# Performance work log

Measured on AMD Instinct MI355X. Metric: run time of the kernel, lower is better.

Reference implementation:

```python
import jax, jax.numpy as jnp
import numpy as np
from jax import lax

# Dense-equivalent of the spconv net: SubMConv/SparseConv with stride 1 and
# size-preserving padding on a dense input reduce to ordinary conv2d.
# Layer chain: (1->64,k1) PReLU (64->256,k3) PReLU (256->512,k3) PReLU
# (512->256,k3) PReLU (256->64,k3) PReLU (64->1,k3) PReLU, then symmetrize.

CHANS = [(1, 64, 1), (64, 256, 3), (256, 512, 3), (512, 256, 3), (256, 64, 3), (64, 1, 3)]


def _conv(x, w, b, k):
    pad = ((k // 2, k // 2), (k // 2, k // 2))
    y = lax.conv_general_dilated(x, w, window_strides=(1, 1), padding=pad,
                                 dimension_numbers=('NCHW', 'OIHW', 'NCHW'))
    return y + b[None, :, None, None]


def _prelu(x, a):
    return jnp.where(x >= 0, x, a * x)


def setup_inputs() -> dict:
    key = jax.random.key(0)
    keys = jax.random.split(key, 1 + 2 * len(CHANS))
    inp = {'A': jax.random.normal(keys[0], (1, 1, 512, 512), dtype=jnp.float32)}
    for i, (cin, cout, k) in enumerate(CHANS):
        fan_in = cin * k * k
        std = 1.0 / np.sqrt(fan_in)
        inp[f'w{i}'] = jax.random.normal(keys[1 + 2 * i], (cout, cin, k, k), dtype=jnp.float32) * std
        inp[f'b{i}'] = jax.random.normal(keys[2 + 2 * i], (cout,), dtype=jnp.float32) * std
        inp[f'p{i}'] = jnp.full((1,), 0.25, dtype=jnp.float32)  # PReLU default weight
    return inp


def reference(A, w0, b0, p0, w1, b1, p1, w2, b2, p2, w3, b3, p3, w4, b4, p4, w5, b5, p5):
    params = [(w0, b0, p0), (w1, b1, p1), (w2, b2, p2), (w3, b3, p3), (w4, b4, p4), (w5, b5, p5)]
    x = A
    for (w, b, p), (_, _, k) in zip(params, CHANS):
        x = _prelu(_conv(x, w, b, k), p)
    # make_symmetric: average with transpose over the spatial (matrix) dims
    return 0.5 * (x + jnp.swapaxes(x, -1, -2))
```

## Files before the change

kernel.cpp:

```cpp
#include <hip/hip_runtime.h>
#include <hip/hip_bf16.h>
#include <stdint.h>

typedef __bf16 bf16_t;
typedef __bf16 bf16x8 __attribute__((ext_vector_type(8)));
typedef float  f32x4  __attribute__((ext_vector_type(4)));

#define HP 514
#define AS1 __attribute__((address_space(1)))
#define AS3 __attribute__((address_space(3)))

__device__ __forceinline__ bf16_t f2bf(float f) { return (bf16_t)f; }

__global__ void l0_kernel(const float* __restrict__ A, const float* __restrict__ w0,
                          const float* __restrict__ b0, const float* __restrict__ p0,
                          bf16_t* __restrict__ X0)
{
    int idx = blockIdx.x * 256 + threadIdx.x;
    if (idx >= HP * HP * 64) return;
    int c   = idx & 63;
    int pix = idx >> 6;
    int py = pix / HP, px = pix - py * HP;
    float v = 0.f;
    if (py >= 1 && py <= 512 && px >= 1 && px <= 512) {
        float a = A[(py - 1) * 512 + (px - 1)];
        v = fmaf(w0[c], a, b0[c]);
        v = v >= 0.f ? v : p0[0] * v;
    }
    X0[idx] = f2bf(v);
}

__global__ void zero_rows_kernel(bf16_t* __restrict__ buf, int C, int r0, int n)
{
    int idx = blockIdx.x * 256 + threadIdx.x;
    int rowsz = HP * C;
    if (idx >= n * rowsz) return;
    int r = idx / rowsz, j = idx - r * rowsz;
    buf[(size_t)(r0 + r) * rowsz + j] = f2bf(0.f);
}

__global__ void zero_cols_kernel(bf16_t* __restrict__ buf, int C, int R)
{
    int idx = blockIdx.x * 256 + threadIdx.x;
    if (idx >= R * 2 * C) return;
    int r = idx / (2 * C);
    int t = idx - r * 2 * C;
    int col = (t < C) ? 0 : 513;
    int c = t % C;
    buf[((size_t)r * HP + col) * C + c] = f2bf(0.f);
}

__global__ void wtrans_kernel(const float* __restrict__ w, bf16_t* __restrict__ wt,
                              int COUT, int CIN)
{
    int idx = blockIdx.x * 256 + threadIdx.x;
    if (idx >= COUT * CIN * 9) return;
    int G    = COUT / 16;
    int j    = idx & 7;
    int l    = (idx >> 3) & 63;
    int t    = idx >> 9;
    int gabs = t % G;
    int t2   = t / G;
    int tap  = t2 % 9;
    int ci   = t2 / 9;
    int cout = gabs * 16 + (l & 15);
    int cin  = ci * 32 + (l >> 4) * 8 + j;
    wt[idx] = f2bf(w[(cout * CIN + cin) * 9 + tap]);
}

template<int CIN, int COUT, int BN>
__global__ __launch_bounds__(256, 3)
void conv3x3_kernel(const bf16_t* __restrict__ in, const bf16_t* __restrict__ wt,
                    const float* __restrict__ bias, const float* __restrict__ alpha,
                    bf16_t* __restrict__ out,
                    int n_rows, int in_off, int in_alloc, int out_off)
{
    constexpr int G      = COUT / 16;
    constexpr int NT     = BN / 32;
    constexpr int NC     = CIN / 32;
    constexpr int AUNITS = 18 * 10 * 4;
    constexpr int APAD   = 768;
    constexpr int ASLAB  = APAD * 8;
    __shared__ __align__(16) bf16_t As[2 * ASLAB];

    const int tid  = threadIdx.x;
    const int lane = tid & 63;
    const int wave = tid >> 6;
    const int lm   = lane & 15;
    const int quad = lane >> 4;
    const int wave_m = wave >> 1;
    const int wave_n = wave & 1;

    const int bid  = blockIdx.x + 64 * (blockIdx.y + gridDim.y * blockIdx.z);
    const int nwg  = 64 * gridDim.y * gridDim.z;
    const int sid  = (bid & 7) * (nwg >> 3) + (bid >> 3);
    const int sx   = sid & 63;
    const int tzy  = sid >> 6;
    const int szb  = tzy % gridDim.z;
    const int syb  = tzy / gridDim.z;

    const int x0 = sx * 8;
    const int y0 = syb * 16;
    const int zb = szb;
    const int gb_blk = zb * (BN / 16);

    int a_srcb[3];
    #pragma unroll
    for (int it = 0; it < 3; ++it) {
        int u  = it * 256 + tid;
        int uu = u < AUNITS ? u : AUNITS - 1;
        int qq = uu & 3, px = (uu >> 2) % 10, r = uu / 40;
        int q  = (qq - (px >> 1)) & 3;
        int grow = in_off + y0 + r;
        grow = grow < 0 ? 0 : (grow >= in_alloc ? in_alloc - 1 : grow);
        a_srcb[it] = (grow * HP + x0 + px) * CIN + q * 8;
    }

    const int pxb = lm & 7, pyb = lm >> 3;
    int sw[3];
    #pragma unroll
    for (int dx = 0; dx < 3; ++dx)
        sw[dx] = ((quad + ((pxb + dx) >> 1)) & 3) * 8;
    int addrA0[4];
    #pragma unroll
    for (int mt = 0; mt < 4; ++mt)
        addrA0[mt] = ((wave_m * 8 + mt * 2 + pyb) * 40 + pxb * 4) * 8;

    auto stageA = [&](int cc, int abuf) {
        #pragma unroll
        for (int it = 0; it < 3; ++it) {
            const bf16_t* src = in + a_srcb[it] + cc;
            bf16_t* dst = As + abuf * ASLAB + (it * 256 + wave * 64) * 8;
            __builtin_amdgcn_global_load_lds((AS1 void*)src, (AS3 void*)dst, 16, 0, 0);
        }
    };
    auto loadB = [&](int ft, bf16x8* b) {
        const bf16_t* base = wt + ((size_t)ft * G + gb_blk + wave_n * NT) * 512 + lane * 8;
        #pragma unroll
        for (int nt = 0; nt < NT; ++nt)
            b[nt] = *(const bf16x8*)(base + nt * 512);
    };
    auto readA = [&](int ab, int tap, bf16x8* a) {
        const int dy = tap / 3, dx = tap - dy * 3;
        const int shift = (dy * 40 + dx * 4) * 8 + sw[dx];
        #pragma unroll
        for (int mt = 0; mt < 4; ++mt)
            a[mt] = *(const bf16x8*)(As + ab * ASLAB + addrA0[mt] + shift);
    };

    f32x4 acc[4][NT] = {};
    bf16x8 breg[2][NT];
    bf16x8 areg[2][4];

    stageA(0, 0);
    loadB(0, breg[0]);
    __syncthreads();
    readA(0, 0, areg[0]);

    for (int cp = 0; cp < NC / 2; ++cp) {
        const bool morecp = (cp + 1 < NC / 2);
        const int fb = cp * 18;
        #pragma unroll
        for (int rf = 0; rf < 18; ++rf) {
            if (rf < 17 || morecp)
                loadB(fb + rf + 1, breg[(rf + 1) & 1]);
            if (rf == 0)            stageA((2 * cp + 1) * 32, 1);
            if (rf == 9 && morecp)  stageA((2 * cp + 2) * 32, 0);
            if (rf != 8 && rf != 17)
                readA((rf + 1) >= 9 ? 1 : 0, (rf + 1) % 9, areg[(rf + 1) & 1]);

            __builtin_amdgcn_s_setprio(1);
            #pragma unroll
            for (int mt = 0; mt < 4; ++mt)
                #pragma unroll
                for (int nt = 0; nt < NT; ++nt)
                    acc[mt][nt] = __builtin_amdgcn_mfma_f32_16x16x32_bf16(
                        areg[rf & 1][mt], breg[rf & 1][nt], acc[mt][nt], 0, 0, 0);
            __builtin_amdgcn_s_setprio(0);

            if (rf == 8) {
                __syncthreads();
                readA(1, 0, areg[1]);
            }
            if (rf == 17 && morecp) {
                __syncthreads();
                readA(0, 0, areg[0]);
            }
        }
    }

    const float al = alpha[0];
    #pragma unroll
    for (int nt = 0; nt < NT; ++nt) {
        const int n = zb * BN + wave_n * (BN / 2) + nt * 16 + lm;
        const float bv = bias[n];
        #pragma unroll
        for (int mt = 0; mt < 4; ++mt) {
            f32x4 v = acc[mt][nt];
            #pragma unroll
            for (int r = 0; r < 4; ++r) {
                int m  = wave_m * 64 + mt * 16 + quad * 4 + r;
                int py = m >> 3, px = m & 7;
                int ly = y0 + py;
                if (ly < n_rows) {
                    float f = v[r] + bv;
                    f = f >= 0.f ? f : al * f;
                    out[((size_t)(out_off + ly) * HP + (x0 + px + 1)) * COUT + n] = f2bf(f);
                }
            }
        }
    }
}

__device__ __forceinline__ float conv64_at(const bf16_t* __restrict__ X,
                                           const float* __restrict__ wsh,
                                           int y, int x, float bv)
{
    float acc = bv;
    #pragma unroll
    for (int dy = 0; dy < 3; ++dy) {
        #pragma unroll
        for (int dx = 0; dx < 3; ++dx) {
            const bf16x8* p = (const bf16x8*)(X + ((size_t)(y + dy) * HP + (x + dx)) * 64);
            const float* wf = wsh + (dy * 3 + dx) * 64;
            #pragma unroll
            for (int j = 0; j < 8; ++j) {
                bf16x8 v = p[j];
                #pragma unroll
                for (int k = 0; k < 8; ++k)
                    acc = fmaf((float)v[k], wf[j * 8 + k], acc);
            }
        }
    }
    return acc;
}

__global__ __launch_bounds__(256)
void l5_strip_kernel(const bf16_t* __restrict__ B4, const bf16_t* __restrict__ wt5,
                     const float* __restrict__ b5, const float* __restrict__ p5,
                     float* __restrict__ T, int abs_row0)
{
    __shared__ float wsh[9 * 64];
    for (int i = threadIdx.x; i < 576; i += 256) wsh[i] = (float)wt5[i];
    __syncthreads();
    int idx = blockIdx.x * 256 + threadIdx.x;
    int ly = idx >> 9, x = idx & 511;
    float bv = b5[0], al = p5[0];
    float t = conv64_at(B4, wsh, ly, x, bv);
    t = t >= 0.f ? t : al * t;
    T[(size_t)(abs_row0 + ly) * 512 + x] = t;
}

__global__ void wtrans5_kernel(const float* __restrict__ w, bf16_t* __restrict__ wt)
{
    int idx = blockIdx.x * 256 + threadIdx.x;
    if (idx >= 9 * 64) return;
    int cin = idx % 64, tap = idx / 64;
    wt[idx] = f2bf(w[cin * 9 + tap]);
}

__global__ __launch_bounds__(256)
void sym_kernel(const float* __restrict__ T, float* __restrict__ out)
{
    int idx = blockIdx.x * 256 + threadIdx.x;
    int y = idx >> 9, x = idx & 511;
    out[idx] = 0.5f * (T[idx] + T[x * 512 + y]);
}

extern "C" void kernel_launch(void* const* d_in, const int* in_sizes, int n_in,
                              void* d_out, int out_size, void* d_ws, size_t ws_size,
                              hipStream_t stream)
{
    const float* A = (const float*)d_in[0];
    const float *w[6], *b[6], *p[6];
    for (int i = 0; i < 6; ++i) {
        w[i] = (const float*)d_in[1 + 3 * i];
        b[i] = (const float*)d_in[2 + 3 * i];
        p[i] = (const float*)d_in[3 + 3 * i];
    }

    auto footprint = [](long long S) -> size_t {
        auto al = [](size_t v) { return (v + 255) & ~(size_t)255; };
        size_t t = 0;
        t += al((size_t)HP * HP * 64 * 2);
        t += al((size_t)(S + 8) * HP * 256 * 2);
        t += al((size_t)(S + 6) * HP * 512 * 2);
        t += al((size_t)(S + 2) * HP * 64 * 2);
        t += al((size_t)512 * 512 * 4);
        t += al((size_t)9 * 256 * 64 * 2);
        t += al((size_t)9 * 512 * 256 * 2);
        t += al((size_t)9 * 256 * 512 * 2);
        t += al((size_t)9 * 64 * 256 * 2);
        t += al((size_t)9 * 64 * 2);
        return t;
    };
    const int cand[6] = {512, 256, 128, 64, 32, 16};
    int S = 16;
    for (int i = 0; i < 6; ++i)
        if (footprint(cand[i]) <= ws_size) { S = cand[i]; break; }
    const int nStrips = 512 / S;

    char* ws = (char*)d_ws;
    size_t off = 0;
    auto carve = [&](size_t bytes) -> void* {
        void* r = ws + off;
        off += (bytes + 255) & ~(size_t)255;
        return r;
    };
    bf16_t* X0  = (bf16_t*)carve((size_t)HP * HP * 64 * 2);
    bf16_t* B1  = (bf16_t*)carve((size_t)(S + 8) * HP * 256 * 2);
    bf16_t* B2  = (bf16_t*)carve((size_t)(S + 6) * HP * 512 * 2);
    bf16_t* B4  = (bf16_t*)carve((size_t)(S + 2) * HP * 64 * 2);
    float*  T   = (float*)carve((size_t)512 * 512 * 4);
    bf16_t* wt1 = (bf16_t*)carve((size_t)9 * 256 * 64 * 2);
    bf16_t* wt2 = (bf16_t*)carve((size_t)9 * 512 * 256 * 2);
    bf16_t* wt3 = (bf16_t*)carve((size_t)9 * 256 * 512 * 2);
    bf16_t* wt4 = (bf16_t*)carve((size_t)9 * 64 * 256 * 2);
    bf16_t* wt5 = (bf16_t*)carve((size_t)9 * 64 * 2);
    bf16_t* B3  = B1;

    auto cdiv = [](int a, int bq) { return (a + bq - 1) / bq; };
    auto zrows = [&](bf16_t* buf, int C, int r0, int n) {
        if (n > 0)
            zero_rows_kernel<<<cdiv(n * HP * C, 256), 256, 0, stream>>>(buf, C, r0, n);
    };

    wtrans_kernel<<<cdiv(9 * 256 * 64, 256), 256, 0, stream>>>(w[1], wt1, 256, 64);
    wtrans_kernel<<<cdiv(9 * 512 * 256, 256), 256, 0, stream>>>(w[2], wt2, 512, 256);
    wtrans_kernel<<<cdiv(9 * 256 * 512, 256), 256, 0, stream>>>(w[3], wt3, 256, 512);
    wtrans_kernel<<<cdiv(9 * 64 * 256, 256), 256, 0, stream>>>(w[4], wt4, 64, 256);
    wtrans5_kernel<<<cdiv(9 * 64, 256), 256, 0, stream>>>(w[5], wt5);
    l0_kernel<<<cdiv(HP * HP * 64, 256), 256, 0, stream>>>(A, w[0], b[0], p[0], X0);
    zero_cols_kernel<<<cdiv((S + 8) * 2 * 256, 256), 256, 0, stream>>>(B1, 256, S + 8);
    zero_cols_kernel<<<cdiv((S + 6) * 2 * 512, 256), 256, 0, stream>>>(B2, 512, S + 6);
    zero_cols_kernel<<<cdiv((S + 2) * 2 * 64, 256), 256, 0, stream>>>(B4, 64, S + 2);

    for (int s = 0; s < nStrips; ++s) {
        const int base = S * s;
        int o0[5], nn[5], ooff[5], alloc[5];
        for (int k = 1; k <= 4; ++k) {
            int hk = 5 - k;
            int a0 = base - hk, a1 = base + S + hk;
            int c0 = a0 < 0 ? 0 : a0, c1 = a1 > 512 ? 512 : a1;
            o0[k] = c0; nn[k] = c1 - c0; ooff[k] = c0 - a0; alloc[k] = S + 2 * hk;
        }
        {
            int in_off = o0[1];
            dim3 g(64, cdiv(nn[1], 16), 2);
            conv3x3_kernel<64, 256, 128><<<g, 256, 0, stream>>>(
                X0, wt1, b[1], p[1], B1, nn[1], in_off, 514, ooff[1]);
            zrows(B1, 256, 0, ooff[1]);
            zrows(B1, 256, ooff[1] + nn[1], alloc[1] - ooff[1] - nn[1]);
        }
        {
            int in_off = (o0[2] - 1) - (base - 4);
            dim3 g(64, cdiv(nn[2], 16), 4);
            conv3x3_kernel<256, 512, 128><<<g, 256, 0, stream>>>(
                B1, wt2, b[2], p[2], B2, nn[2], in_off, alloc[1], ooff[2]);
            zrows(B2, 512, 0, ooff[2]);
            zrows(B2, 512, ooff[2] + nn[2], alloc[2] - ooff[2] - nn[2]);
        }
        {
            int in_off = (o0[3] - 1) - (base - 3);
            dim3 g(64, cdiv(nn[3], 16), 2);
            conv3x3_kernel<512, 256, 128><<<g, 256, 0, stream>>>(
                B2, wt3, b[3], p[3], B3, nn[3], in_off, alloc[2], ooff[3]);
            zrows(B3, 256, 0, ooff[3]);
            zrows(B3, 256, ooff[3] + nn[3], alloc[3] - ooff[3] - nn[3]);
        }
        {
            int in_off = (o0[4] - 1) - (base - 2);
            dim3 g(64, cdiv(nn[4], 16), 1);
            conv3x3_kernel<256, 64, 64><<<g, 256, 0, stream>>>(
                B3, wt4, b[4], p[4], B4, nn[4], in_off, alloc[3], ooff[4]);
            zrows(B4, 64, 0, ooff[4]);
            zrows(B4, 64, ooff[4] + nn[4], alloc[4] - ooff[4] - nn[4]);
        }
        l5_strip_kernel<<<(S * 512) / 256, 256, 0, stream>>>(B4, wt5, b[5], p[5], T, base);
    }

    sym_kernel<<<(512 * 512) / 256, 256, 0, stream>>>(T, (float*)d_out);
}
```

Before: 1.445 ms.

## Stage conv epilogue through swizzled LDS for 16-byte coalesced output stores

The conv3x3 epilogue now writes bias+PReLU results into a swizzled shared-memory tile, reusing the A staging buffer, then copies them out with 16-byte vector stores per pixel instead of scattered 2-byte bf16 stores. This is meant to cut the number of global store transactions and improve coalescing. The block-to-tile mapping also changes so the channel block (z) varies fastest in the swizzled id, using a shift and mask that assume gridDim.z is a power of two. The cost is two extra barriers and an LDS round trip.

```diff
diff --git a/kernel.cpp b/kernel.cpp
--- a/kernel.cpp
+++ b/kernel.cpp
@@ -81,7 +81,11 @@
     constexpr int AUNITS = 18 * 10 * 4;
     constexpr int APAD   = 768;
     constexpr int ASLAB  = APAD * 8;
-    __shared__ __align__(16) bf16_t As[2 * ASLAB];
+    constexpr int ROWB   = BN * 2;
+    constexpr int SMASK  = ROWB / 32 - 1;
+    constexpr int SMEM_B = (2 * ASLAB * 2 > 128 * ROWB) ? 2 * ASLAB * 2 : 128 * ROWB;
+    __shared__ __align__(16) char smem[SMEM_B];
+    bf16_t* As = (bf16_t*)smem;
 
     const int tid  = threadIdx.x;
     const int lane = tid & 63;
@@ -94,10 +98,11 @@
     const int bid  = blockIdx.x + 64 * (blockIdx.y + gridDim.y * blockIdx.z);
     const int nwg  = 64 * gridDim.y * gridDim.z;
     const int sid  = (bid & 7) * (nwg >> 3) + (bid >> 3);
-    const int sx   = sid & 63;
-    const int tzy  = sid >> 6;
-    const int szb  = tzy % gridDim.z;
-    const int syb  = tzy / gridDim.z;
+    const int zsh  = __ffs(gridDim.z) - 1;
+    const int szb  = sid & (gridDim.z - 1);
+    const int t2   = sid >> zsh;
+    const int sx   = t2 & 63;
+    const int syb  = t2 >> 6;
 
     const int x0 = sx * 8;
     const int y0 = syb * 16;
@@ -189,26 +194,39 @@
         }
     }
 
+    __syncthreads();
     const float al = alpha[0];
     #pragma unroll
     for (int nt = 0; nt < NT; ++nt) {
-        const int n = zb * BN + wave_n * (BN / 2) + nt * 16 + lm;
-        const float bv = bias[n];
+        const int c  = wave_n * (BN / 2) + nt * 16 + lm;
+        const float bv = bias[zb * BN + c];
         #pragma unroll
         for (int mt = 0; mt < 4; ++mt) {
             f32x4 v = acc[mt][nt];
             #pragma unroll
             for (int r = 0; r < 4; ++r) {
-                int m  = wave_m * 64 + mt * 16 + quad * 4 + r;
-                int py = m >> 3, px = m & 7;
-                int ly = y0 + py;
-                if (ly < n_rows) {
-                    float f = v[r] + bv;
-                    f = f >= 0.f ? f : al * f;
-                    out[((size_t)(out_off + ly) * HP + (x0 + px + 1)) * COUT + n] = f2bf(f);
-                }
+                int m = wave_m * 64 + mt * 16 + quad * 4 + r;
+                float f = v[r] + bv;
+                f = f >= 0.f ? f : al * f;
+                int byte = m * ROWB + ((c * 2) ^ ((m & SMASK) << 5));
+                *(bf16_t*)(smem + byte) = f2bf(f);
             }
         }
+    }
+    __syncthreads();
+    constexpr int CPI  = ROWB / 16;
+    constexpr int ITER = (128 * CPI) / 256;
+    #pragma unroll
+    for (int i = 0; i < ITER; ++i) {
+        int g = i * 256 + tid;
+        int p = g / CPI;
+        int k = g & (CPI - 1);
+        int sbyte = p * ROWB + ((k * 16) ^ ((p & SMASK) << 5));
+        bf16x8 v16 = *(const bf16x8*)(smem + sbyte);
+        int py = p >> 3, px = p & 7, ly = y0 + py;
+        if (ly < n_rows)
+            *(bf16x8*)(out + ((size_t)(out_off + ly) * HP + (x0 + px + 1)) * COUT
+                       + zb * BN + k * 8) = v16;
     }
 }
 
```

Result: faster. 1.365 ms, median of 3 (-5.5%).
